# Performance work log

Hardware: AMD Instinct MI355X
Metric: run time of the kernel (lower is better)

The kernel has to match this reference:

```python
import jax, jax.numpy as jnp
import numpy as np

B, C, S, F = 128, 5, 512, 3
U = 256          # encoder units
RU = 2 * U       # decoder units / bidirectional encoder width


def _lstm_cell(x_t, h, c, Wk, Wr, b):
    # Keras LSTM gate order: i, f, g(cell), o
    z = x_t @ Wk + h @ Wr + b
    i, f, g, o = jnp.split(z, 4, axis=-1)
    c_new = jax.nn.sigmoid(f) * c + jax.nn.sigmoid(i) * jnp.tanh(g)
    h_new = jax.nn.sigmoid(o) * jnp.tanh(c_new)
    return h_new, c_new


def _masked_lstm(xs, mask, Wk, Wr, b, units):
    # xs: [B,S,D], mask: [B,S] bool. Keras semantics: masked steps carry
    # previous state and previous output (== previous h for LSTM).
    Bn = xs.shape[0]

    def step(carry, inp):
        h, c = carry
        x_t, m_t = inp
        h_n, c_n = _lstm_cell(x_t, h, c, Wk, Wr, b)
        m = m_t[:, None]
        h2 = jnp.where(m, h_n, h)
        c2 = jnp.where(m, c_n, c)
        return (h2, c2), h2

    init = (jnp.zeros((Bn, units), xs.dtype), jnp.zeros((Bn, units), xs.dtype))
    _, outs = jax.lax.scan(step, init, (jnp.swapaxes(xs, 0, 1), mask.T))
    return jnp.swapaxes(outs, 0, 1)  # [B,S,units]


def setup_inputs() -> dict:
    key = jax.random.key(0)
    k = jax.random.split(key, 10)
    s = 0.05
    rn = lambda kk, sh: jax.random.normal(kk, sh, jnp.float32) * s
    return {
        "x": jax.random.normal(k[0], (B, C, S, F), jnp.float32),
        "Wf_k": rn(k[1], (C, 4 * U)), "Wf_r": rn(k[2], (U, 4 * U)), "bf": jnp.zeros((4 * U,), jnp.float32),
        "Wb_k": rn(k[3], (C, 4 * U)), "Wb_r": rn(k[4], (U, 4 * U)), "bb": jnp.zeros((4 * U,), jnp.float32),
        "Wd_k": rn(k[5], (C, 4 * RU)), "Wd_r": rn(k[6], (RU, 4 * RU)), "bd": jnp.zeros((4 * RU,), jnp.float32),
        "W_attn": rn(k[7], (RU + C, 1)), "b_attn": jnp.zeros((1,), jnp.float32),
        "W_dense": rn(k[8], (RU + RU, C)), "b_dense": jnp.zeros((C,), jnp.float32),
    }


def reference(x, Wf_k, Wf_r, bf, Wb_k, Wb_r, bb, Wd_k, Wd_r, bd,
              W_attn, b_attn, W_dense, b_dense):
    xt = jnp.transpose(x, (0, 2, 1, 3))          # [B,S,C,F]
    mask = xt[:, :, 0, 2] != 0                   # tf.cast(..., bool)
    xs = xt[:, :, :, 0]                          # [B,S,C]

    fwd = _masked_lstm(xs, mask, Wf_k, Wf_r, bf, U)
    bwd = _masked_lstm(xs[:, ::-1], mask[:, ::-1], Wb_k, Wb_r, bb, U)[:, ::-1]
    enc = jnp.concatenate([fwd, bwd], axis=-1)   # [B,S,RU]

    # attention(concat([tile(x_t), enc])) is linear -> split the weight:
    Wx, We = W_attn[:C, 0], W_attn[C:, 0]
    enc_scores = jnp.einsum('bsd,d->bs', enc, We) + b_attn[0]  # [B,S]

    hidden0 = enc[:, -1, :]                      # [B,RU]
    x0 = xs[:, 0, :]                             # [B,C]

    def dec_step(carry, _):
        hidden, x_t = carry
        scores = enc_scores + (x_t @ Wx)[:, None]             # [B,S]
        alpha = jax.nn.softmax(scores, axis=1)
        attn = jnp.einsum('bs,bsd->bd', alpha, enc)           # [B,RU]
        # decoder LSTM on a single timestep, initial_state=[hidden, attn]
        h_new, _c = _lstm_cell(x_t, hidden, attn, Wd_k, Wd_r, bd)
        x_new = jnp.concatenate([h_new, attn], axis=-1) @ W_dense + b_dense
        return (h_new, x_new), x_new

    _, ys = jax.lax.scan(dec_step, (hidden0, x0), None, length=S - 1)  # [S-1,B,C]
    return jnp.transpose(ys, (1, 2, 0))[..., None]           # [B,C,S-1,1]
```

## Files before the change

### kernel.cpp

```cpp
#include <hip/hip_runtime.h>
#include <math.h>

#define BATCH 128
#define CCH 5
#define SEQ 512
#define UNITS 256
#define RU 512

#define ENC_N 33554432

__device__ __forceinline__ float sigmoidf_(float v) {
    return 1.0f / (1.0f + __expf(-v));
}
__device__ __forceinline__ float tanhf_(float v) {
    float e = __expf(2.0f * v);
    return 1.0f - 2.0f / (e + 1.0f);
}
__device__ __forceinline__ void astoref(float* p, float v) {
    __hip_atomic_store(p, v, __ATOMIC_RELAXED, __HIP_MEMORY_SCOPE_AGENT);
}
__device__ __forceinline__ void astorei(int* p, int v) {
    __hip_atomic_store(p, v, __ATOMIC_RELAXED, __HIP_MEMORY_SCOPE_AGENT);
}
__device__ __forceinline__ unsigned long long aloadu64(const unsigned long long* p) {
    return __hip_atomic_load(p, __ATOMIC_RELAXED, __HIP_MEMORY_SCOPE_AGENT);
}
__device__ __forceinline__ int aloadi(const int* p) {
    return __hip_atomic_load(p, __ATOMIC_RELAXED, __HIP_MEMORY_SCOPE_AGENT);
}

__global__ __attribute__((amdgpu_flat_work_group_size(1024, 1024),
                          amdgpu_waves_per_eu(4, 4)))
void encoder_kernel(const float* __restrict__ x,
                    const float* __restrict__ Wf_k, const float* __restrict__ Wf_r,
                    const float* __restrict__ bf,
                    const float* __restrict__ Wb_k, const float* __restrict__ Wb_r,
                    const float* __restrict__ bb,
                    float* __restrict__ enc, float* __restrict__ h_ex,
                    int* __restrict__ flags)
{
    const int bid  = blockIdx.x;
    const int dir  = bid >> 7;
    const int tile = (bid >> 3) & 15;
    const int jsl  = bid & 7;
    const int grp  = dir * 16 + tile;
    const int bg0  = tile * 8;
    const float* __restrict__ Wk   = dir ? Wb_k : Wf_k;
    const float* __restrict__ Wr   = dir ? Wb_r : Wf_r;
    const float* __restrict__ bias = dir ? bb : bf;
    const int tid  = threadIdx.x;
    const int wv   = tid >> 6;
    const int lane = tid & 63;
    const int g0 = ((lane >> 5) << 8) + jsl * 32 + (lane & 31);

    __shared__ float2 zpP[16][8][64];
    __shared__ float __align__(16) hLe[2][8][260];
    __shared__ float zred[8][128];
    __shared__ float WkL[5][128];
    __shared__ float biasL[128];
    __shared__ unsigned char mL[8][SEQ];
    __shared__ float xLe[8][8];
    __shared__ int msync;

    for (int i = tid; i < 2 * 8 * 260; i += 1024) ((float*)hLe)[i] = 0.0f;
    if (tid == 0) msync = 0;
    if (tid < 128) biasL[tid] = bias[((tid >> 5) << 8) + jsl * 32 + (tid & 31)];
    if (tid >= 128 && tid < 768) {
        int i = tid - 128, c = i >> 7, cl = i & 127;
        WkL[c][cl] = Wk[c * 1024 + ((cl >> 5) << 8) + jsl * 32 + (cl & 31)];
    }
    for (int i = tid; i < 8 * SEQ; i += 1024) {
        int b = i >> 9, tt = i & (SEQ - 1);
        mL[b][tt] = (x[((size_t)((bg0 + b) * CCH) * SEQ + tt) * 3 + 2] != 0.0f) ? 1 : 0;
    }
    float wr0[16], wr1[16];
    {
        const float* wbase = Wr + (size_t)(wv * 16) * 1024 + g0;
        #pragma unroll
        for (int r = 0; r < 16; ++r) {
            wr0[r] = wbase[(size_t)r * 1024];
            wr1[r] = wbase[(size_t)r * 1024 + 512];
        }
        #pragma unroll
        for (int r = 0; r < 16; ++r)
            asm volatile("" : "+v"(wr0[r]), "+v"(wr1[r]));
    }
    float creg = 0.0f;
    __syncthreads();

    for (int t = 0; t < SEQ; ++t) {
        const int cur = t & 1;
        const int ts = dir ? (SEQ - 1 - t) : t;
        if (t > 0 && wv < 8) {
            const int* fp = &flags[(grp * 8 + wv) * 32];
            if (lane == 0) {
                int guard = 0;
                while (aloadi(fp) < t && guard < (1 << 26)) {
                    __builtin_amdgcn_s_sleep(1); ++guard;
                }
            }
            int b = lane >> 3, u = wv * 32 + (lane & 7) * 4;
            const unsigned long long* hsrc = (const unsigned long long*)
                &h_ex[(size_t)(dir * 2 + ((t - 1) & 1)) * (BATCH * UNITS)
                      + (size_t)(bg0 + b) * UNITS + u];
            unsigned long long v0 = aloadu64(hsrc);
            unsigned long long v1 = aloadu64(hsrc + 1);
            *(unsigned long long*)&hLe[cur][b][u]     = v0;
            *(unsigned long long*)&hLe[cur][b][u + 2] = v1;
        }
        if (tid >= 960 && tid < 1000) {
            int i = tid - 960, b = i / 5, c = i - b * 5;
            xLe[b][c] = x[((size_t)((bg0 + b) * CCH + c) * SEQ + ts) * 3];
        }
        __syncthreads();

        float accA[8], accB[8];
        #pragma unroll
        for (int b = 0; b < 8; ++b) {
            float a0 = 0.f, a1 = 0.f;
            const float4* hp = (const float4*)&hLe[cur][b][wv * 16];
            #pragma unroll
            for (int q = 0; q < 4; ++q) {
                float4 h4 = hp[q];
                a0 = fmaf(h4.x, wr0[4*q+0], a0); a1 = fmaf(h4.x, wr1[4*q+0], a1);
                a0 = fmaf(h4.y, wr0[4*q+1], a0); a1 = fmaf(h4.y, wr1[4*q+1], a1);
                a0 = fmaf(h4.z, wr0[4*q+2], a0); a1 = fmaf(h4.z, wr1[4*q+2], a1);
                a0 = fmaf(h4.w, wr0[4*q+3], a0); a1 = fmaf(h4.w, wr1[4*q+3], a1);
            }
            accA[b] = a0; accB[b] = a1;
        }
        #pragma unroll
        for (int b = 0; b < 8; ++b)
            zpP[wv][b][lane] = make_float2(accA[b], accB[b]);
        __syncthreads();

        {
            int b = tid >> 7, cl = tid & 127;
            int gate = cl >> 5, u = cl & 31;
            int lane_r = ((gate & 1) << 5) | u;
            int comp = gate >> 1;
            const float* zf = (const float*)zpP + b * 128 + lane_r * 2 + comp;
            float sum = biasL[cl];
            #pragma unroll
            for (int s = 0; s < 16; ++s) sum += zf[s * 1024];
            #pragma unroll
            for (int c = 0; c < 5; ++c) sum = fmaf(xLe[b][c], WkL[c][cl], sum);
            zred[b][cl] = sum;
        }
        __syncthreads();

        if (tid < 256) {
            int b = tid >> 5, u = tid & 31;
            float zi = zred[b][u];
            float zf_ = zred[b][32 + u];
            float zg = zred[b][64 + u];
            float zo = zred[b][96 + u];
            float cn = sigmoidf_(zf_) * creg + sigmoidf_(zi) * tanhf_(zg);
            float hn = sigmoidf_(zo) * tanhf_(cn);
            float hprev = hLe[cur][b][jsl * 32 + u];
            float h2 = mL[b][ts] ? hn : hprev;
            float c2 = mL[b][ts] ? cn : creg;
            creg = c2;
            astoref(&h_ex[(size_t)(dir * 2 + (t & 1)) * (BATCH * UNITS)
                          + (size_t)(bg0 + b) * UNITS + jsl * 32 + u], h2);
            enc[((size_t)(bg0 + b) * SEQ + ts) * RU + dir * UNITS + jsl * 32 + u] = h2;
            if (lane == 0) {
                asm volatile("s_waitcnt vmcnt(0)" ::: "memory");
                __hip_atomic_fetch_add(&msync, 1, __ATOMIC_RELAXED,
                                       __HIP_MEMORY_SCOPE_WORKGROUP);
            }
            if (tid == 0) {
                int target = 4 * (t + 1), guard = 0;
                while (__hip_atomic_load(&msync, __ATOMIC_RELAXED,
                                         __HIP_MEMORY_SCOPE_WORKGROUP) < target &&
                       guard < (1 << 26)) ++guard;
                astorei(&flags[(grp * 8 + jsl) * 32], t + 1);
            }
        }
    }
}

__global__ __launch_bounds__(256)
void attn_kernel(const float* __restrict__ enc,
                 const float* __restrict__ W_attn, const float* __restrict__ b_attn,
                 const float* __restrict__ W_dense, const float* __restrict__ b_dense,
                 const float* __restrict__ x,
                 float* __restrict__ attn_ws, float* __restrict__ hidden_ws,
                 float* __restrict__ xbuf, float* __restrict__ xconst)
{
    const int b = blockIdx.x;
    const int tid = threadIdx.x;
    const int lane = tid & 63;
    const int wv = tid >> 6;

    __shared__ float WeL[RU];
    __shared__ float scoresL[SEQ];
    __shared__ float red[256];
    __shared__ float attnL[RU];

    WeL[tid]       = W_attn[CCH + tid];
    WeL[tid + 256] = W_attn[CCH + tid + 256];
    __syncthreads();

    const float* __restrict__ encb = enc + (size_t)b * SEQ * RU;
    const float batt = b_attn[0];

    for (int s = wv; s < SEQ; s += 4) {
        const float* row = encb + (size_t)s * RU;
        float p = 0.0f;
        #pragma unroll
        for (int i = 0; i < 8; ++i) {
            int d = lane * 8 + i;
            p = fmaf(row[d], WeL[d], p);
        }
        #pragma unroll
        for (int o = 32; o; o >>= 1) p += __shfl_xor(p, o);
        if (lane == 0) scoresL[s] = p + batt;
    }
    __syncthreads();

    float m = fmaxf(scoresL[tid], scoresL[tid + 256]);
    red[tid] = m;
    __syncthreads();
    for (int st = 128; st; st >>= 1) {
        if (tid < st) red[tid] = fmaxf(red[tid], red[tid + st]);
        __syncthreads();
    }
    const float mx = red[0];
    __syncthreads();
    float e0 = __expf(scoresL[tid] - mx);
    float e1 = __expf(scoresL[tid + 256] - mx);
    red[tid] = e0 + e1;
    __syncthreads();
    for (int st = 128; st; st >>= 1) {
        if (tid < st) red[tid] += red[tid + st];
        __syncthreads();
    }
    const float sinv = 1.0f / red[0];
    __syncthreads();
    scoresL[tid]       = e0 * sinv;
    scoresL[tid + 256] = e1 * sinv;
    __syncthreads();

    float a0 = 0.0f, a1 = 0.0f;
    for (int s = 0; s < SEQ; ++s) {
        float al = scoresL[s];
        a0 = fmaf(al, encb[(size_t)s * RU + tid], a0);
        a1 = fmaf(al, encb[(size_t)s * RU + tid + 256], a1);
    }
    attn_ws[(size_t)b * RU + tid]       = a0;
    attn_ws[(size_t)b * RU + tid + 256] = a1;
    attnL[tid] = a0;
    attnL[tid + 256] = a1;
    hidden_ws[(size_t)b * RU + tid]       = encb[(size_t)(SEQ - 1) * RU + tid];
    hidden_ws[(size_t)b * RU + tid + 256] = encb[(size_t)(SEQ - 1) * RU + tid + 256];
    if (tid < CCH) xbuf[b * CCH + tid] = x[((size_t)(b * CCH + tid) * SEQ + 0) * 3];
    __syncthreads();

    if (tid < CCH) {
        float acc = b_dense[tid];
        for (int d = 0; d < RU; ++d)
            acc = fmaf(attnL[d], W_dense[(RU + d) * CCH + tid], acc);
        xconst[b * CCH + tid] = acc;
    }
}

__global__ __attribute__((amdgpu_flat_work_group_size(1024, 1024),
                          amdgpu_waves_per_eu(4, 4)))
void decoder_kernel(const float* __restrict__ Wd_k, const float* __restrict__ Wd_r,
                    const float* __restrict__ bd,
                    const float* __restrict__ W_dense,
                    const float* __restrict__ attn_ws, const float* __restrict__ hidden_ws,
                    const float* __restrict__ xbuf, const float* __restrict__ xconst,
                    float* __restrict__ h_ex, int* __restrict__ flags,
                    float* __restrict__ out)
{
    const int bid  = blockIdx.x;
    const int tile = bid >> 4;
    const int jsl  = bid & 15;
    const int bg0  = tile * 8;
    const int tid  = threadIdx.x;
    const int wv   = tid >> 6;
    const int lane = tid & 63;
    const int g0 = ((lane >> 5) << 9) + jsl * 32 + (lane & 31);

    __shared__ float2 zpP[16][8][64];
    __shared__ float __align__(16) hLd[2][8][516];
    __shared__ float zred[8][128];
    __shared__ float WdL[RU * CCH];
    __shared__ float WkL[5][128];
    __shared__ float biasL[128];
    __shared__ float attL[8][32];
    __shared__ float xL[8][8], xcL[8][8];
    __shared__ int msync;

    for (int i = tid; i < RU * CCH; i += 1024) WdL[i] = W_dense[i];
    if (tid == 0) msync = 0;
    if (tid < 128) biasL[tid] = bd[((tid >> 5) << 9) + jsl * 32 + (tid & 31)];
    if (tid >= 128 && tid < 768) {
        int i = tid - 128, c = i >> 7, cl = i & 127;
        WkL[c][cl] = Wd_k[c * 2048 + ((cl >> 5) << 9) + jsl * 32 + (cl & 31)];
    }
    if (tid < 256) {
        int b = tid >> 5, u = tid & 31;
        attL[b][u] = attn_ws[(size_t)(bg0 + b) * RU + jsl * 32 + u];
    }
    if (tid < 64) {
        int b = tid >> 3, c = tid & 7;
        if (c < 5) {
            xL[b][c]  = xbuf[(bg0 + b) * CCH + c];
            xcL[b][c] = xconst[(bg0 + b) * CCH + c];
        }
    }
    {
        int f = tid * 4, b = f >> 9, u = f & (RU - 1);
        float4 v = *(const float4*)&hidden_ws[(size_t)(bg0 + b) * RU + u];
        *(float4*)&hLd[0][b][u] = v;
    }
    float wr0[32], wr1[32];
    {
        const float* wbase = Wd_r + (size_t)(wv * 32) * 2048 + g0;
        #pragma unroll
        for (int r = 0; r < 32; ++r) {
            wr0[r] = wbase[(size_t)r * 2048];
            wr1[r] = wbase[(size_t)r * 2048 + 1024];
        }
        #pragma unroll
        for (int r = 0; r < 32; ++r)
            asm volatile("" : "+v"(wr0[r]), "+v"(wr1[r]));
    }
    __syncthreads();

    for (int t = 0; t < SEQ - 1; ++t) {
        const int cur = t & 1;
        if (t > 0) {
            const int* fp = &flags[(tile * 16 + wv) * 32];
            if (lane == 0) {
                int guard = 0;
                while (aloadi(fp) < t && guard < (1 << 26)) {
                    __builtin_amdgcn_s_sleep(1); ++guard;
                }
            }
            int b = lane >> 3, u = wv * 32 + (lane & 7) * 4;
            const unsigned long long* hsrc = (const unsigned long long*)
                &h_ex[(size_t)((t - 1) & 1) * (BATCH * RU)
                      + (size_t)(bg0 + b) * RU + u];
            unsigned long long v0 = aloadu64(hsrc);
            unsigned long long v1 = aloadu64(hsrc + 1);
            *(unsigned long long*)&hLd[cur][b][u]     = v0;
            *(unsigned long long*)&hLd[cur][b][u + 2] = v1;
        }
        __syncthreads();

        float accA[8], accB[8];
        #pragma unroll
        for (int b = 0; b < 8; ++b) {
            float a0 = 0.f, a1 = 0.f;
            const float4* hp = (const float4*)&hLd[cur][b][wv * 32];
            #pragma unroll
            for (int q = 0; q < 8; ++q) {
                float4 h4 = hp[q];
                a0 = fmaf(h4.x, wr0[4*q+0], a0); a1 = fmaf(h4.x, wr1[4*q+0], a1);
                a0 = fmaf(h4.y, wr0[4*q+1], a0); a1 = fmaf(h4.y, wr1[4*q+1], a1);
                a0 = fmaf(h4.z, wr0[4*q+2], a0); a1 = fmaf(h4.z, wr1[4*q+2], a1);
                a0 = fmaf(h4.w, wr0[4*q+3], a0); a1 = fmaf(h4.w, wr1[4*q+3], a1);
            }
            accA[b] = a0; accB[b] = a1;
        }
        #pragma unroll
        for (int b = 0; b < 8; ++b)
            zpP[wv][b][lane] = make_float2(accA[b], accB[b]);

        if (t > 0) {
            for (int it = wv; it < 40; it += 16) {
                int bb = it / 5, c = it - bb * 5;
                float p = 0.f;
                #pragma unroll
                for (int q = 0; q < 8; ++q) {
                    int uu = lane + (q << 6);
                    p = fmaf(hLd[cur][bb][uu], WdL[uu * CCH + c], p);
                }
                #pragma unroll
                for (int o = 32; o; o >>= 1) p += __shfl_xor(p, o);
                if (lane == 0) xL[bb][c] = p + xcL[bb][c];
            }
        }
        __syncthreads();

        {
            int b = tid >> 7, cl = tid & 127;
            int gate = cl >> 5, u = cl & 31;
            int lane_r = ((gate & 1) << 5) | u;
            int comp = gate >> 1;
            const float* zf = (const float*)zpP + b * 128 + lane_r * 2 + comp;
            float sum = biasL[cl];
            #pragma unroll
            for (int s = 0; s < 16; ++s) sum += zf[s * 1024];
            #pragma unroll
            for (int c = 0; c < 5; ++c) sum = fmaf(xL[b][c], WkL[c][cl], sum);
            zred[b][cl] = sum;
        }
        __syncthreads();

        if (tid < 256) {
            int b = tid >> 5, u = tid & 31;
            float zi = zred[b][u];
            float zf_ = zred[b][32 + u];
            float zg = zred[b][64 + u];
            float zo = zred[b][96 + u];
            float cn = sigmoidf_(zf_) * attL[b][u] + sigmoidf_(zi) * tanhf_(zg);
            float hn = sigmoidf_(zo) * tanhf_(cn);
            astoref(&h_ex[(size_t)(t & 1) * (BATCH * RU)
                          + (size_t)(bg0 + b) * RU + jsl * 32 + u], hn);
            if (lane == 0) {
                asm volatile("s_waitcnt vmcnt(0)" ::: "memory");
                __hip_atomic_fetch_add(&msync, 1, __ATOMIC_RELAXED,
                                       __HIP_MEMORY_SCOPE_WORKGROUP);
            }
            if (tid == 0) {
                int target = 4 * (t + 1), guard = 0;
                while (__hip_atomic_load(&msync, __ATOMIC_RELAXED,
                                         __HIP_MEMORY_SCOPE_WORKGROUP) < target &&
                       guard < (1 << 26)) ++guard;
                astorei(&flags[(tile * 16 + jsl) * 32], t + 1);
            }
        }
        if (t > 0 && jsl == 0 && tid >= 256 && tid < 296) {
            int i = tid - 256, bb = i / 5, c = i - bb * 5;
            out[(size_t)((bg0 + bb) * CCH + c) * (SEQ - 1) + (t - 1)] = xL[bb][c];
        }
    }

    {
        const int t = SEQ - 1;
        const int cur = t & 1;
        const int* fp = &flags[(tile * 16 + wv) * 32];
        if (lane == 0) {
            int guard = 0;
            while (aloadi(fp) < t && guard < (1 << 26)) {
                __builtin_amdgcn_s_sleep(1); ++guard;
            }
        }
        int b = lane >> 3, u = wv * 32 + (lane & 7) * 4;
        const unsigned long long* hsrc = (const unsigned long long*)
            &h_ex[(size_t)((t - 1) & 1) * (BATCH * RU)
                  + (size_t)(bg0 + b) * RU + u];
        unsigned long long v0 = aloadu64(hsrc);
        unsigned long long v1 = aloadu64(hsrc + 1);
        *(unsigned long long*)&hLd[cur][b][u]     = v0;
        *(unsigned long long*)&hLd[cur][b][u + 2] = v1;
        __syncthreads();
        if (jsl == 0) {
            for (int it = wv; it < 40; it += 16) {
                int bb = it / 5, c = it - bb * 5;
                float p = 0.f;
                #pragma unroll
                for (int q = 0; q < 8; ++q) {
                    int uu = lane + (q << 6);
                    p = fmaf(hLd[cur][bb][uu], WdL[uu * CCH + c], p);
                }
                #pragma unroll
                for (int o = 32; o; o >>= 1) p += __shfl_xor(p, o);
                if (lane == 0)
                    out[(size_t)((bg0 + bb) * CCH + c) * (SEQ - 1) + (t - 1)]
                        = p + xcL[bb][c];
            }
        }
    }
}

extern "C" void kernel_launch(void* const* d_in, const int* in_sizes, int n_in,
                              void* d_out, int out_size, void* d_ws, size_t ws_size,
                              hipStream_t stream)
{
    const float* x       = (const float*)d_in[0];
    const float* Wf_k    = (const float*)d_in[1];
    const float* Wf_r    = (const float*)d_in[2];
    const float* bf      = (const float*)d_in[3];
    const float* Wb_k    = (const float*)d_in[4];
    const float* Wb_r    = (const float*)d_in[5];
    const float* bb      = (const float*)d_in[6];
    const float* Wd_k    = (const float*)d_in[7];
    const float* Wd_r    = (const float*)d_in[8];
    const float* bd      = (const float*)d_in[9];
    const float* W_attn  = (const float*)d_in[10];
    const float* b_attn  = (const float*)d_in[11];
    const float* W_dense = (const float*)d_in[12];
    const float* b_dense = (const float*)d_in[13];
    float* out = (float*)d_out;

    float* ws = (float*)d_ws;
    float* enc      = ws;
    float* attn_p   = ws + ENC_N;
    float* hidden_p = ws + ENC_N + 65536;
    float* xbuf_p   = ws + ENC_N + 131072;
    float* xconst_p = ws + ENC_N + 131712;
    float* h_ex_e   = ws + ENC_N;
    int*   flag_e   = (int*)(ws + ENC_N + 131072);
    int*   flag_d   = (int*)ws;
    float* h_ex_d   = ws + 8192;

    hipMemsetAsync(flag_e, 0, 8192 * sizeof(int), stream);
    encoder_kernel<<<256, 1024, 0, stream>>>(x, Wf_k, Wf_r, bf, Wb_k, Wb_r, bb,
                                             enc, h_ex_e, flag_e);
    attn_kernel<<<BATCH, 256, 0, stream>>>(enc, W_attn, b_attn, W_dense, b_dense, x,
                                           attn_p, hidden_p, xbuf_p, xconst_p);
    hipMemsetAsync(flag_d, 0, 8192 * sizeof(int), stream);
    decoder_kernel<<<256, 1024, 0, stream>>>(Wd_k, Wd_r, bd, W_dense,
                                             attn_p, hidden_p, xbuf_p, xconst_p,
                                             h_ex_d, flag_d, out);
}
```

Measured before the change: 6.396 ms.

## Replace intra-block msync counter with per-wave flags and simplify partial-sum layout

Drops the shared-memory atomic counter that tid 0 spun on before publishing the step flag. Each of the four writer waves now sets its own flag slot, and consumers poll four slots with four lanes. Partial sums move from an interleaved float2 layout to a plain [16][8][128] layout with direct indexing. The previous h and the attention cell state are kept in registers. In the decoder the dense-output projection moves ahead of the recurrent matvec, and the final-step tail is restricted to jsl==0 blocks. The aim is to shorten the critical path of each recurrent step, at the cost of more flag polling traffic.

```diff
diff --git a/kernel.cpp b/kernel.cpp
--- a/kernel.cpp
+++ b/kernel.cpp
@@ -48,22 +48,20 @@
     const float* __restrict__ Wk   = dir ? Wb_k : Wf_k;
     const float* __restrict__ Wr   = dir ? Wb_r : Wf_r;
     const float* __restrict__ bias = dir ? bb : bf;
-    const int tid  = threadIdx.x;
-    const int wv   = tid >> 6;
-    const int lane = tid & 63;
-    const int g0 = ((lane >> 5) << 8) + jsl * 32 + (lane & 31);
-
-    __shared__ float2 zpP[16][8][64];
+    const int tid = threadIdx.x;
+    const int wv  = tid >> 6;
+    const int l   = tid & 63;
+    const int g0 = ((l >> 5) << 8) + jsl * 32 + (l & 31);
+
+    __shared__ float zp[16][8][128];
     __shared__ float __align__(16) hLe[2][8][260];
     __shared__ float zred[8][128];
     __shared__ float WkL[5][128];
     __shared__ float biasL[128];
     __shared__ unsigned char mL[8][SEQ];
     __shared__ float xLe[8][8];
-    __shared__ int msync;
 
     for (int i = tid; i < 2 * 8 * 260; i += 1024) ((float*)hLe)[i] = 0.0f;
-    if (tid == 0) msync = 0;
     if (tid < 128) biasL[tid] = bias[((tid >> 5) << 8) + jsl * 32 + (tid & 31)];
     if (tid >= 128 && tid < 768) {
         int i = tid - 128, c = i >> 7, cl = i & 127;
@@ -85,28 +83,30 @@
         for (int r = 0; r < 16; ++r)
             asm volatile("" : "+v"(wr0[r]), "+v"(wr1[r]));
     }
-    float creg = 0.0f;
+    float creg = 0.0f, hreg = 0.0f;
     __syncthreads();
 
     for (int t = 0; t < SEQ; ++t) {
         const int cur = t & 1;
         const int ts = dir ? (SEQ - 1 - t) : t;
         if (t > 0 && wv < 8) {
-            const int* fp = &flags[(grp * 8 + wv) * 32];
-            if (lane == 0) {
+            if (l < 4) {
+                const int* fp = &flags[(grp * 8 + wv) * 32 + l];
                 int guard = 0;
                 while (aloadi(fp) < t && guard < (1 << 26)) {
                     __builtin_amdgcn_s_sleep(1); ++guard;
                 }
             }
-            int b = lane >> 3, u = wv * 32 + (lane & 7) * 4;
+            int b = l >> 3, u0 = wv * 32 + (l & 7) * 4;
             const unsigned long long* hsrc = (const unsigned long long*)
-                &h_ex[(size_t)(dir * 2 + ((t - 1) & 1)) * (BATCH * UNITS)
-                      + (size_t)(bg0 + b) * UNITS + u];
+                &h_ex[(size_t)(dir * 2 + ((t - 1) & 1)) * 32768
+                      + (size_t)(bg0 + b) * UNITS + u0];
             unsigned long long v0 = aloadu64(hsrc);
             unsigned long long v1 = aloadu64(hsrc + 1);
-            *(unsigned long long*)&hLe[cur][b][u]     = v0;
-            *(unsigned long long*)&hLe[cur][b][u + 2] = v1;
+            float4 hv;
+            ((unsigned long long*)&hv)[0] = v0;
+            ((unsigned long long*)&hv)[1] = v1;
+            *(float4*)&hLe[cur][b][u0] = hv;
         }
         if (tid >= 960 && tid < 1000) {
             int i = tid - 960, b = i / 5, c = i - b * 5;
@@ -130,19 +130,17 @@
             accA[b] = a0; accB[b] = a1;
         }
         #pragma unroll
-        for (int b = 0; b < 8; ++b)
-            zpP[wv][b][lane] = make_float2(accA[b], accB[b]);
+        for (int b = 0; b < 8; ++b) {
+            zp[wv][b][l]      = accA[b];
+            zp[wv][b][64 + l] = accB[b];
+        }
         __syncthreads();
 
         {
             int b = tid >> 7, cl = tid & 127;
-            int gate = cl >> 5, u = cl & 31;
-            int lane_r = ((gate & 1) << 5) | u;
-            int comp = gate >> 1;
-            const float* zf = (const float*)zpP + b * 128 + lane_r * 2 + comp;
             float sum = biasL[cl];
             #pragma unroll
-            for (int s = 0; s < 16; ++s) sum += zf[s * 1024];
+            for (int s = 0; s < 16; ++s) sum += zp[s][b][cl];
             #pragma unroll
             for (int c = 0; c < 5; ++c) sum = fmaf(xLe[b][c], WkL[c][cl], sum);
             zred[b][cl] = sum;
@@ -152,30 +150,20 @@
         if (tid < 256) {
             int b = tid >> 5, u = tid & 31;
             float zi = zred[b][u];
-            float zf_ = zred[b][32 + u];
+            float zf = zred[b][32 + u];
             float zg = zred[b][64 + u];
             float zo = zred[b][96 + u];
-            float cn = sigmoidf_(zf_) * creg + sigmoidf_(zi) * tanhf_(zg);
+            float cn = sigmoidf_(zf) * creg + sigmoidf_(zi) * tanhf_(zg);
             float hn = sigmoidf_(zo) * tanhf_(cn);
-            float hprev = hLe[cur][b][jsl * 32 + u];
-            float h2 = mL[b][ts] ? hn : hprev;
-            float c2 = mL[b][ts] ? cn : creg;
-            creg = c2;
-            astoref(&h_ex[(size_t)(dir * 2 + (t & 1)) * (BATCH * UNITS)
+            int m = mL[b][ts];
+            float h2 = m ? hn : hreg;
+            float c2 = m ? cn : creg;
+            creg = c2; hreg = h2;
+            astoref(&h_ex[(size_t)(dir * 2 + cur) * 32768
                           + (size_t)(bg0 + b) * UNITS + jsl * 32 + u], h2);
             enc[((size_t)(bg0 + b) * SEQ + ts) * RU + dir * UNITS + jsl * 32 + u] = h2;
-            if (lane == 0) {
-                asm volatile("s_waitcnt vmcnt(0)" ::: "memory");
-                __hip_atomic_fetch_add(&msync, 1, __ATOMIC_RELAXED,
-                                       __HIP_MEMORY_SCOPE_WORKGROUP);
-            }
-            if (tid == 0) {
-                int target = 4 * (t + 1), guard = 0;
-                while (__hip_atomic_load(&msync, __ATOMIC_RELAXED,
-                                         __HIP_MEMORY_SCOPE_WORKGROUP) < target &&
-                       guard < (1 << 26)) ++guard;
-                astorei(&flags[(grp * 8 + jsl) * 32], t + 1);
-            }
+            asm volatile("s_waitcnt vmcnt(0)" ::: "memory");
+            if (l == 0) astorei(&flags[(grp * 8 + jsl) * 32 + wv], t + 1);
         }
     }
 }
@@ -281,29 +269,22 @@
     const int bg0  = tile * 8;
     const int tid  = threadIdx.x;
     const int wv   = tid >> 6;
-    const int lane = tid & 63;
-    const int g0 = ((lane >> 5) << 9) + jsl * 32 + (lane & 31);
-
-    __shared__ float2 zpP[16][8][64];
-    __shared__ float __align__(16) hLd[2][8][516];
+    const int l    = tid & 63;
+    const int g0 = ((l >> 5) << 9) + jsl * 32 + (l & 31);
+
+    __shared__ float zp[16][8][128];
+    __shared__ float __align__(16) hL[2][8][516];
     __shared__ float zred[8][128];
     __shared__ float WdL[RU * CCH];
     __shared__ float WkL[5][128];
     __shared__ float biasL[128];
-    __shared__ float attL[8][32];
     __shared__ float xL[8][8], xcL[8][8];
-    __shared__ int msync;
 
     for (int i = tid; i < RU * CCH; i += 1024) WdL[i] = W_dense[i];
-    if (tid == 0) msync = 0;
     if (tid < 128) biasL[tid] = bd[((tid >> 5) << 9) + jsl * 32 + (tid & 31)];
     if (tid >= 128 && tid < 768) {
         int i = tid - 128, c = i >> 7, cl = i & 127;
         WkL[c][cl] = Wd_k[c * 2048 + ((cl >> 5) << 9) + jsl * 32 + (cl & 31)];
-    }
-    if (tid < 256) {
-        int b = tid >> 5, u = tid & 31;
-        attL[b][u] = attn_ws[(size_t)(bg0 + b) * RU + jsl * 32 + u];
     }
     if (tid < 64) {
         int b = tid >> 3, c = tid & 7;
@@ -314,9 +295,11 @@
     }
     {
         int f = tid * 4, b = f >> 9, u = f & (RU - 1);
-        float4 v = *(const float4*)&hidden_ws[(size_t)(bg0 + b) * RU + u];
-        *(float4*)&hLd[0][b][u] = v;
-    }
+        *(float4*)&hL[0][b][u] = *(const float4*)&hidden_ws[(size_t)(bg0 + b) * RU + u];
+    }
+    float attR = 0.0f;
+    if (tid < 256)
+        attR = attn_ws[(size_t)(bg0 + (tid >> 5)) * RU + jsl * 32 + (tid & 31)];
     float wr0[32], wr1[32];
     {
         const float* wbase = Wd_r + (size_t)(wv * 32) * 2048 + g0;
@@ -334,29 +317,45 @@
     for (int t = 0; t < SEQ - 1; ++t) {
         const int cur = t & 1;
         if (t > 0) {
-            const int* fp = &flags[(tile * 16 + wv) * 32];
-            if (lane == 0) {
+            if (l < 4) {
+                const int* fp = &flags[(tile * 16 + wv) * 32 + l];
                 int guard = 0;
                 while (aloadi(fp) < t && guard < (1 << 26)) {
                     __builtin_amdgcn_s_sleep(1); ++guard;
                 }
             }
-            int b = lane >> 3, u = wv * 32 + (lane & 7) * 4;
+            int b = l >> 3, u0 = wv * 32 + (l & 7) * 4;
             const unsigned long long* hsrc = (const unsigned long long*)
-                &h_ex[(size_t)((t - 1) & 1) * (BATCH * RU)
-                      + (size_t)(bg0 + b) * RU + u];
+                &h_ex[(size_t)((t - 1) & 1) * 65536 + (size_t)(bg0 + b) * RU + u0];
             unsigned long long v0 = aloadu64(hsrc);
             unsigned long long v1 = aloadu64(hsrc + 1);
-            *(unsigned long long*)&hLd[cur][b][u]     = v0;
-            *(unsigned long long*)&hLd[cur][b][u + 2] = v1;
-        }
-        __syncthreads();
+            float4 hv;
+            ((unsigned long long*)&hv)[0] = v0;
+            ((unsigned long long*)&hv)[1] = v1;
+            *(float4*)&hL[cur][b][u0] = hv;
+        }
+        __syncthreads();
+
+        if (t > 0) {
+            for (int it = wv; it < 40; it += 16) {
+                int bb = it / 5, c = it - bb * 5;
+                float p = 0.f;
+                #pragma unroll
+                for (int q = 0; q < 8; ++q) {
+                    int uu = l + (q << 6);
+                    p = fmaf(hL[cur][bb][uu], WdL[uu * CCH + c], p);
+                }
+                #pragma unroll
+                for (int o = 32; o; o >>= 1) p += __shfl_xor(p, o);
+                if (l == 0) xL[bb][c] = p + xcL[bb][c];
+            }
+        }
 
         float accA[8], accB[8];
         #pragma unroll
         for (int b = 0; b < 8; ++b) {
             float a0 = 0.f, a1 = 0.f;
-            const float4* hp = (const float4*)&hLd[cur][b][wv * 32];
+            const float4* hp = (const float4*)&hL[cur][b][wv * 32];
             #pragma unroll
             for (int q = 0; q < 8; ++q) {
                 float4 h4 = hp[q];
@@ -368,34 +367,17 @@
             accA[b] = a0; accB[b] = a1;
         }
         #pragma unroll
-        for (int b = 0; b < 8; ++b)
-            zpP[wv][b][lane] = make_float2(accA[b], accB[b]);
-
-        if (t > 0) {
-            for (int it = wv; it < 40; it += 16) {
-                int bb = it / 5, c = it - bb * 5;
-                float p = 0.f;
-                #pragma unroll
-                for (int q = 0; q < 8; ++q) {
-                    int uu = lane + (q << 6);
-                    p = fmaf(hLd[cur][bb][uu], WdL[uu * CCH + c], p);
-                }
-                #pragma unroll
-                for (int o = 32; o; o >>= 1) p += __shfl_xor(p, o);
-                if (lane == 0) xL[bb][c] = p + xcL[bb][c];
-            }
+        for (int b = 0; b < 8; ++b) {
+            zp[wv][b][l]      = accA[b];
+            zp[wv][b][64 + l] = accB[b];
         }
         __syncthreads();
 
         {
             int b = tid >> 7, cl = tid & 127;
-            int gate = cl >> 5, u = cl & 31;
-            int lane_r = ((gate & 1) << 5) | u;
-            int comp = gate >> 1;
-            const float* zf = (const float*)zpP + b * 128 + lane_r * 2 + comp;
             float sum = biasL[cl];
             #pragma unroll
-            for (int s = 0; s < 16; ++s) sum += zf[s * 1024];
+            for (int s = 0; s < 16; ++s) sum += zp[s][b][cl];
             #pragma unroll
             for (int c = 0; c < 5; ++c) sum = fmaf(xL[b][c], WkL[c][cl], sum);
             zred[b][cl] = sum;
@@ -405,25 +387,15 @@
         if (tid < 256) {
             int b = tid >> 5, u = tid & 31;
             float zi = zred[b][u];
-            float zf_ = zred[b][32 + u];
+            float zf = zred[b][32 + u];
             float zg = zred[b][64 + u];
             float zo = zred[b][96 + u];
-            float cn = sigmoidf_(zf_) * attL[b][u] + sigmoidf_(zi) * tanhf_(zg);
+            float cn = sigmoidf_(zf) * attR + sigmoidf_(zi) * tanhf_(zg);
             float hn = sigmoidf_(zo) * tanhf_(cn);
-            astoref(&h_ex[(size_t)(t & 1) * (BATCH * RU)
+            astoref(&h_ex[(size_t)cur * 65536
                           + (size_t)(bg0 + b) * RU + jsl * 32 + u], hn);
-            if (lane == 0) {
-                asm volatile("s_waitcnt vmcnt(0)" ::: "memory");
-                __hip_atomic_fetch_add(&msync, 1, __ATOMIC_RELAXED,
-                                       __HIP_MEMORY_SCOPE_WORKGROUP);
-            }
-            if (tid == 0) {
-                int target = 4 * (t + 1), guard = 0;
-                while (__hip_atomic_load(&msync, __ATOMIC_RELAXED,
-                                         __HIP_MEMORY_SCOPE_WORKGROUP) < target &&
-                       guard < (1 << 26)) ++guard;
-                astorei(&flags[(tile * 16 + jsl) * 32], t + 1);
-            }
+            asm volatile("s_waitcnt vmcnt(0)" ::: "memory");
+            if (l == 0) astorei(&flags[(tile * 16 + jsl) * 32 + wv], t + 1);
         }
         if (t > 0 && jsl == 0 && tid >= 256 && tid < 296) {
             int i = tid - 256, bb = i / 5, c = i - bb * 5;
@@ -431,40 +403,39 @@
         }
     }
 
-    {
+    if (jsl == 0) {
         const int t = SEQ - 1;
         const int cur = t & 1;
-        const int* fp = &flags[(tile * 16 + wv) * 32];
-        if (lane == 0) {
+        if (l < 4) {
+            const int* fp = &flags[(tile * 16 + wv) * 32 + l];
             int guard = 0;
             while (aloadi(fp) < t && guard < (1 << 26)) {
                 __builtin_amdgcn_s_sleep(1); ++guard;
             }
         }
-        int b = lane >> 3, u = wv * 32 + (lane & 7) * 4;
+        int b = l >> 3, u0 = wv * 32 + (l & 7) * 4;
         const unsigned long long* hsrc = (const unsigned long long*)
-            &h_ex[(size_t)((t - 1) & 1) * (BATCH * RU)
-                  + (size_t)(bg0 + b) * RU + u];
+            &h_ex[(size_t)((t - 1) & 1) * 65536 + (size_t)(bg0 + b) * RU + u0];
         unsigned long long v0 = aloadu64(hsrc);
         unsigned long long v1 = aloadu64(hsrc + 1);
-        *(unsigned long long*)&hLd[cur][b][u]     = v0;
-        *(unsigned long long*)&hLd[cur][b][u + 2] = v1;
-        __syncthreads();
-        if (jsl == 0) {
-            for (int it = wv; it < 40; it += 16) {
-                int bb = it / 5, c = it - bb * 5;
-                float p = 0.f;
-                #pragma unroll
-                for (int q = 0; q < 8; ++q) {
-                    int uu = lane + (q << 6);
-                    p = fmaf(hLd[cur][bb][uu], WdL[uu * CCH + c], p);
-                }
-                #pragma unroll
-                for (int o = 32; o; o >>= 1) p += __shfl_xor(p, o);
-                if (lane == 0)
-                    out[(size_t)((bg0 + bb) * CCH + c) * (SEQ - 1) + (t - 1)]
-                        = p + xcL[bb][c];
-            }
+        float4 hv;
+        ((unsigned long long*)&hv)[0] = v0;
+        ((unsigned long long*)&hv)[1] = v1;
+        *(float4*)&hL[cur][b][u0] = hv;
+        __syncthreads();
+        for (int it = wv; it < 40; it += 16) {
+            int bb = it / 5, c = it - bb * 5;
+            float p = 0.f;
+            #pragma unroll
+            for (int q = 0; q < 8; ++q) {
+                int uu = l + (q << 6);
+                p = fmaf(hL[cur][bb][uu], WdL[uu * CCH + c], p);
+            }
+            #pragma unroll
+            for (int o = 32; o; o >>= 1) p += __shfl_xor(p, o);
+            if (l == 0)
+                out[(size_t)((bg0 + bb) * CCH + c) * (SEQ - 1) + (t - 1)]
+                    = p + xcL[bb][c];
         }
     }
 }
```

Measured after the change: 5.736 ms. 1.12x faster.
